# Performance work log

Hardware: AMD Instinct MI355X
Metric: run time of the kernel (lower is better)

Reference implementation:

```python
import jax, jax.numpy as jnp
import numpy as np

B, T, D, H, L, K, DFF = 8, 512, 512, 8, 4, 31, 2048
DK = D // H
PAD = (K - 1) // 2

def _ln(x, g, b, eps=1e-5):
    m = x.mean(-1, keepdims=True)
    v = ((x - m) ** 2).mean(-1, keepdims=True)
    return (x - m) * jax.lax.rsqrt(v + eps) * g + b

def _swish(x):
    return x * jax.nn.sigmoid(x)

def _rel_shift(x):
    # x: [B,H,T,P] with P = 2T-1 (Transformer-XL style shift)
    b, h, q, p = x.shape
    x = jnp.pad(x, ((0, 0), (0, 0), (0, 0), (1, 0)))
    x = x.reshape(b, h, p + 1, q)[:, :, 1:].reshape(b, h, q, p)
    return x

def setup_inputs() -> dict:
    key = jax.random.key(0)
    ks = iter(jax.random.split(key, 64))
    def w(shape, s=0.02):
        return jax.random.normal(next(ks), shape, jnp.float32) * s
    inp = {
        'x': jax.random.normal(next(ks), (B, T, D), jnp.float32),
        'pos_emb': jax.random.normal(next(ks), (1, 2 * T - 1, D), jnp.float32),
        'ln1_g': jnp.ones((L, D)), 'ln1_b': jnp.zeros((L, D)),
        'ff1_w1': w((L, D, DFF)), 'ff1_b1': jnp.zeros((L, DFF)),
        'ff1_w2': w((L, DFF, D)), 'ff1_b2': jnp.zeros((L, D)),
        'lnA_g': jnp.ones((L, D)), 'lnA_b': jnp.zeros((L, D)),
        'Wq': w((L, D, D)), 'bq': jnp.zeros((L, D)),
        'Wk': w((L, D, D)), 'bk': jnp.zeros((L, D)),
        'Wv': w((L, D, D)), 'bv': jnp.zeros((L, D)),
        'Wo': w((L, D, D)), 'bo': jnp.zeros((L, D)),
        'Wpos': w((L, D, D)),
        'pbu': jnp.zeros((L, H, DK)), 'pbv': jnp.zeros((L, H, DK)),
        'lnC_g': jnp.ones((L, D)), 'lnC_b': jnp.zeros((L, D)),
        'pw1_w': w((L, 2 * D, D)), 'pw1_b': jnp.zeros((L, 2 * D)),
        'dw_w': w((L, D, K)), 'dw_b': jnp.zeros((L, D)),
        'cln_g': jnp.ones((L, D)), 'cln_b': jnp.zeros((L, D)),
        'pw2_w': w((L, D, D)), 'pw2_b': jnp.zeros((L, D)),
        'ln2_g': jnp.ones((L, D)), 'ln2_b': jnp.zeros((L, D)),
        'ff2_w1': w((L, D, DFF)), 'ff2_b1': jnp.zeros((L, DFF)),
        'ff2_w2': w((L, DFF, D)), 'ff2_b2': jnp.zeros((L, D)),
        'lnO_g': jnp.ones((L, D)), 'lnO_b': jnp.zeros((L, D)),
    }
    return inp

def reference(x, pos_emb, ln1_g, ln1_b, ff1_w1, ff1_b1, ff1_w2, ff1_b2,
              lnA_g, lnA_b, Wq, bq, Wk, bk, Wv, bv, Wo, bo, Wpos, pbu, pbv,
              lnC_g, lnC_b, pw1_w, pw1_b, dw_w, dw_b, cln_g, cln_b, pw2_w, pw2_b,
              ln2_g, ln2_b, ff2_w1, ff2_b1, ff2_w2, ff2_b2, lnO_g, lnO_b):
    scale = 1.0 / np.sqrt(DK).astype(np.float32)
    for i in range(L):
        # FFN 1 (half-step residual)
        res = x
        y = _ln(x, ln1_g[i], ln1_b[i])
        y = _swish(y @ ff1_w1[i] + ff1_b1[i]) @ ff1_w2[i] + ff1_b2[i]
        res = res + 0.5 * y
        # rel-pos multi-head self-attention
        y = _ln(res, lnA_g[i], lnA_b[i])
        q = (y @ Wq[i] + bq[i]).reshape(B, T, H, DK)
        k = (y @ Wk[i] + bk[i]).reshape(B, T, H, DK)
        v = (y @ Wv[i] + bv[i]).reshape(B, T, H, DK)
        p = (pos_emb @ Wpos[i]).reshape(1, 2 * T - 1, H, DK)
        ac = jnp.einsum('bthd,bshd->bhts', q + pbu[i], k)          # content score
        bd = jnp.einsum('bthd,xshd->bhts', q + pbv[i], p)          # position score
        bd = _rel_shift(bd)[..., :T]
        attn = jax.nn.softmax((ac + bd) * scale, axis=-1)
        o = jnp.einsum('bhts,bshd->bthd', attn, v).reshape(B, T, D)
        res = res + (o @ Wo[i] + bo[i])
        # convolution module
        y = _ln(res, lnC_g[i], lnC_b[i])
        y = y @ pw1_w[i].T + pw1_b[i]                               # (B,T,2D)
        a, g = jnp.split(y, 2, axis=-1)
        y = a * jax.nn.sigmoid(g)                                   # GLU over channels
        y = jax.lax.conv_general_dilated(
            y.transpose(0, 2, 1), dw_w[i][:, None, :],
            window_strides=(1,), padding=[(PAD, PAD)],
            feature_group_count=D,
            dimension_numbers=('NCH', 'OIH', 'NCH'))
        y = y.transpose(0, 2, 1) + dw_b[i]                          # (B,T,D)
        y = _swish(_ln(y, cln_g[i], cln_b[i]))
        y = y @ pw2_w[i].T + pw2_b[i]
        res = res + y
        # FFN 2 (half-step residual)
        y = _ln(res, ln2_g[i], ln2_b[i])
        y = _swish(y @ ff2_w1[i] + ff2_b1[i]) @ ff2_w2[i] + ff2_b2[i]
        res = res + 0.5 * y
        x = _ln(res, lnO_g[i], lnO_b[i])
    return x
```

## Files before the change

kernel.cpp:

```cpp
#include <hip/hip_runtime.h>


typedef unsigned short u16;
typedef unsigned int u32;
typedef __attribute__((ext_vector_type(8))) short bf16x8;
typedef __attribute__((ext_vector_type(4))) float f32x4;

#define DI __device__ __forceinline__

constexpr int CT = 512;
constexpr int CD = 512;
constexpr int CH = 8;
constexpr int CDK = 64;
constexpr int CDFF = 2048;
constexpr int CNBT = 4096;
constexpr int CL = 4;

DI u16 f2bf(float f) {
  u32 u = __builtin_bit_cast(u32, f);
  u = u + 0x7fffu + ((u >> 16) & 1u);
  return (u16)(u >> 16);
}
DI float bf2f(u16 h) { u32 u = ((u32)h) << 16; return __builtin_bit_cast(float, u); }
DI u32 pack2(float a, float b) { return (u32)f2bf(a) | ((u32)f2bf(b) << 16); }
DI float sigm(float x) { return 1.0f / (1.0f + __expf(-x)); }

DI f32x4 MFMA(bf16x8 a, bf16x8 b, f32x4 c) {
  return __builtin_amdgcn_mfma_f32_16x16x32_bf16(a, b, c, 0, 0, 0);
}

DI void gload16(const void* g, void* l) {
  __builtin_amdgcn_global_load_lds((const __attribute__((address_space(1))) void*)g,
                                   (__attribute__((address_space(3))) void*)l, 16, 0, 0);
}

DI float wsum(float v) {
#pragma unroll
  for (int o = 32; o > 0; o >>= 1) v += __shfl_xor(v, o, 64);
  return v;
}

DI void tbody(const float* ip, u16* op, int R, int C, int c0, int r0,
              int tx, int ty) {
  __shared__ float t[32][33];
#pragma unroll
  for (int i = ty; i < 32; i += 8)
    t[i][tx] = ip[(long)(r0 + i) * C + c0 + tx];
  __syncthreads();
#pragma unroll
  for (int i = ty; i < 32; i += 8)
    op[(long)(c0 + i) * R + r0 + tx] = f2bf(t[tx][i]);
}

__global__ __launch_bounds__(256) void tconv2x_k(const float* __restrict__ in0,
                                                 const float* __restrict__ in1,
                                                 u16* __restrict__ out0,
                                                 u16* __restrict__ out1,
                                                 int R, int C) {
  int z = blockIdx.z;
  int l = z & 3;
  const float* ip = (z < 4 ? in0 : in1) + (long)l * R * C;
  u16* op = (z < 4 ? out0 : out1) + (long)l * R * C;
  tbody(ip, op, R, C, blockIdx.x * 32, blockIdx.y * 32, threadIdx.x, threadIdx.y);
}

__global__ __launch_bounds__(256) void tconvQ_k(
    const float* __restrict__ Wq, const float* __restrict__ Wk,
    const float* __restrict__ Wv, const float* __restrict__ Wo,
    const float* __restrict__ Wpos, u16* __restrict__ wt_qkv,
    u16* __restrict__ wt_o, u16* __restrict__ wt_pos) {
  int z = blockIdx.z;
  int sel = z >> 2, l = z & 3;
  const float* ip;
  u16* op;
  const long S = 512L * 512;
  switch (sel) {
    case 0: ip = Wq + l * S; op = wt_qkv + (long)l * 1536 * 512; break;
    case 1: ip = Wk + l * S; op = wt_qkv + (long)l * 1536 * 512 + S; break;
    case 2: ip = Wv + l * S; op = wt_qkv + (long)l * 1536 * 512 + 2 * S; break;
    case 3: ip = Wo + l * S; op = wt_o + l * S; break;
    default: ip = Wpos + l * S; op = wt_pos + l * S; break;
  }
  tbody(ip, op, 512, 512, blockIdx.x * 32, blockIdx.y * 32, threadIdx.x, threadIdx.y);
}

__global__ __launch_bounds__(256) void cvt_k(const float* __restrict__ in,
                                             u16* __restrict__ out, long nIn, long nOut,
                                             long inZ, long outZ) {
  long i = ((long)blockIdx.x * 256 + threadIdx.x) * 4;
  if (i >= nOut) return;
  const float* ip = in + (long)blockIdx.y * inZ;
  u16* op = out + (long)blockIdx.y * outZ;
  u16 o[4];
#pragma unroll
  for (int j = 0; j < 4; ++j) {
    long idx = i + j;
    o[j] = (idx < nIn) ? f2bf(ip[idx]) : (u16)0;
  }
  uint2 st;
  st.x = (u32)o[0] | ((u32)o[1] << 16);
  st.y = (u32)o[2] | ((u32)o[3] << 16);
  *(uint2*)&op[i] = st;
}

__global__ __launch_bounds__(256) void pwperm_k(const float* __restrict__ in,
                                                u16* __restrict__ out) {
  int l = blockIdx.y;
  long i = (long)blockIdx.x * 256 + threadIdx.x;
  long n = i >> 7;
  int c = (int)(i & 127) * 4;
  int q = (int)(n >> 4) & 1;
  long r = (q ? 512 : 0) + ((n >> 5) << 4) + (n & 15);
  const float* ip = in + ((long)l * 1024 + r) * 512 + c;
  float4 v = *(const float4*)ip;
  u16* op = out + ((long)l * 1024 + n) * 512 + c;
  uint2 st;
  st.x = pack2(v.x, v.y);
  st.y = pack2(v.z, v.w);
  *(uint2*)op = st;
}

__global__ __launch_bounds__(256) void setup3_k(
    const float* __restrict__ in_pos, u16* __restrict__ posbf,
    const float* __restrict__ dw_w, float* __restrict__ dwT,
    const float* __restrict__ bq, const float* __restrict__ bk,
    const float* __restrict__ bv, float* __restrict__ qkvb) {
  int y = blockIdx.y;
  long x = blockIdx.x;
  int tid = threadIdx.x;
  if (y == 0) {
    long i = (x * 256 + tid) * 4;
    const long nIn = 1023L * 512, nOut = 1024L * 512;
    if (i >= nOut) return;
    u16 o[4];
#pragma unroll
    for (int j = 0; j < 4; ++j) {
      long idx = i + j;
      o[j] = (idx < nIn) ? f2bf(in_pos[idx]) : (u16)0;
    }
    uint2 st;
    st.x = (u32)o[0] | ((u32)o[1] << 16);
    st.y = (u32)o[2] | ((u32)o[3] << 16);
    *(uint2*)&posbf[i] = st;
  } else if (y == 1) {
    long idx = x * 256 + tid;
    if (idx >= 4L * 31 * 512) return;
    long l = idx / (31 * 512);
    int rem = (int)(idx % (31 * 512));
    int k = rem >> 9, d = rem & 511;
    dwT[idx] = dw_w[l * 512 * 31 + d * 31 + k];
  } else {
    long idx = x * 256 + tid;
    if (idx >= 4L * 1536) return;
    int z = (int)(idx / 1536), j = (int)(idx % 1536);
    float v;
    if (j < 512) v = bq[z * 512 + j];
    else if (j < 1024) v = bk[z * 512 + j - 512];
    else v = bv[z * 512 + j - 1024];
    qkvb[idx] = v;
  }
}

template <int F32OUT>
__global__ __launch_bounds__(256) void ln_k(const float* in, void* out,
                                            const float* gw, const float* bw) {
  int tid = threadIdx.x, wid = tid >> 6, lane = tid & 63;
  long row = (long)blockIdx.x * 4 + wid;
  const float* x = in + row * CD + lane * 8;
  float4 v0 = *(const float4*)x;
  float4 v1 = *(const float4*)(x + 4);
  float s = v0.x + v0.y + v0.z + v0.w + v1.x + v1.y + v1.z + v1.w;
  float q = v0.x * v0.x + v0.y * v0.y + v0.z * v0.z + v0.w * v0.w +
            v1.x * v1.x + v1.y * v1.y + v1.z * v1.z + v1.w * v1.w;
  s = wsum(s);
  q = wsum(q);
  float mean = s * (1.0f / CD);
  float var = q * (1.0f / CD) - mean * mean;
  float rs = rsqrtf(var + 1e-5f);
  int c = lane * 8;
  float4 g0 = *(const float4*)(gw + c), g1 = *(const float4*)(gw + c + 4);
  float4 b0 = *(const float4*)(bw + c), b1 = *(const float4*)(bw + c + 4);
  float y0 = (v0.x - mean) * rs * g0.x + b0.x;
  float y1 = (v0.y - mean) * rs * g0.y + b0.y;
  float y2 = (v0.z - mean) * rs * g0.z + b0.z;
  float y3 = (v0.w - mean) * rs * g0.w + b0.w;
  float y4 = (v1.x - mean) * rs * g1.x + b1.x;
  float y5 = (v1.y - mean) * rs * g1.y + b1.y;
  float y6 = (v1.z - mean) * rs * g1.z + b1.z;
  float y7 = (v1.w - mean) * rs * g1.w + b1.w;
  if (F32OUT) {
    float* o = (float*)out + row * CD + c;
    *(float4*)o = make_float4(y0, y1, y2, y3);
    *(float4*)(o + 4) = make_float4(y4, y5, y6, y7);
  } else {
    u16* o = (u16*)out + row * CD + c;
    uint4 pk;
    pk.x = pack2(y0, y1);
    pk.y = pack2(y2, y3);
    pk.z = pack2(y4, y5);
    pk.w = pack2(y6, y7);
    *(uint4*)o = pk;
  }
}

__global__ __launch_bounds__(256) void ln_cp_k(const float* __restrict__ in,
                                               float* __restrict__ cur,
                                               u16* __restrict__ ybf,
                                               const float* gw, const float* bw) {
  int tid = threadIdx.x, wid = tid >> 6, lane = tid & 63;
  long row = (long)blockIdx.x * 4 + wid;
  const float* x = in + row * CD + lane * 8;
  float v[8];
  *(float4*)&v[0] = *(const float4*)x;
  *(float4*)&v[4] = *(const float4*)(x + 4);
  float* cx = cur + row * CD + lane * 8;
  *(float4*)cx = *(float4*)&v[0];
  *(float4*)(cx + 4) = *(float4*)&v[4];
  float s = 0.f, q = 0.f;
#pragma unroll
  for (int j = 0; j < 8; ++j) { s += v[j]; q += v[j] * v[j]; }
  s = wsum(s);
  q = wsum(q);
  float mean = s * (1.0f / CD);
  float var = q * (1.0f / CD) - mean * mean;
  float rs = rsqrtf(var + 1e-5f);
  int c = lane * 8;
  float y[8];
#pragma unroll
  for (int j = 0; j < 8; ++j) y[j] = (v[j] - mean) * rs * gw[c + j] + bw[c + j];
  u16* o = ybf + row * CD + c;
  uint4 pk;
  pk.x = pack2(y[0], y[1]);
  pk.y = pack2(y[2], y[3]);
  pk.z = pack2(y[4], y[5]);
  pk.w = pack2(y[6], y[7]);
  *(uint4*)o = pk;
}

__global__ __launch_bounds__(256) void lnln_k(float* cur, u16* ybf,
                                              const float* gO, const float* bO,
                                              const float* g1, const float* b1) {
  int tid = threadIdx.x, wid = tid >> 6, lane = tid & 63;
  long row = (long)blockIdx.x * 4 + wid;
  float* x = cur + row * CD + lane * 8;
  float v[8];
  *(float4*)&v[0] = *(const float4*)x;
  *(float4*)&v[4] = *(const float4*)(x + 4);
  float s = 0.f, q = 0.f;
#pragma unroll
  for (int j = 0; j < 8; ++j) { s += v[j]; q += v[j] * v[j]; }
  s = wsum(s);
  q = wsum(q);
  float mean = s * (1.0f / CD);
  float var = q * (1.0f / CD) - mean * mean;
  float rs = rsqrtf(var + 1e-5f);
  int c = lane * 8;
  float y[8];
#pragma unroll
  for (int j = 0; j < 8; ++j) y[j] = (v[j] - mean) * rs * gO[c + j] + bO[c + j];
  *(float4*)x = *(float4*)&y[0];
  *(float4*)(x + 4) = *(float4*)&y[4];
  float s2 = 0.f, q2 = 0.f;
#pragma unroll
  for (int j = 0; j < 8; ++j) { s2 += y[j]; q2 += y[j] * y[j]; }
  s2 = wsum(s2);
  q2 = wsum(q2);
  float mean2 = s2 * (1.0f / CD);
  float var2 = q2 * (1.0f / CD) - mean2 * mean2;
  float rs2 = rsqrtf(var2 + 1e-5f);
  float z[8];
#pragma unroll
  for (int j = 0; j < 8; ++j) z[j] = (y[j] - mean2) * rs2 * g1[c + j] + b1[c + j];
  u16* o = ybf + row * CD + c;
  uint4 pk;
  pk.x = pack2(z[0], z[1]);
  pk.y = pack2(z[2], z[3]);
  pk.z = pack2(z[4], z[5]);
  pk.w = pack2(z[6], z[7]);
  *(uint4*)o = pk;
}

template <int EPI, int SPLITK>
__global__ __launch_bounds__(256, 2) void gemm2_k(
    const u16* __restrict__ A, const u16* __restrict__ B, void* C,
    const float* __restrict__ bias, float alpha, int lda, int ldb, int ldc, int Kd) {
  __shared__ u16 lds[3][2][64 * 64];
  const int tid = threadIdx.x, wid = tid >> 6, lane = tid & 63;
  const int m0 = blockIdx.x * 64, n0 = blockIdx.y * 64;
  const int wm = wid >> 1, wn = wid & 1;
  const int fr = lane & 15, fq = lane >> 4;
  const f32x4 vz = {0.f, 0.f, 0.f, 0.f};
  f32x4 acc[2][2] = {{vz, vz}, {vz, vz}};

  const int Kc = Kd / SPLITK;
  const int kb0 = (SPLITK > 1) ? blockIdx.z * Kc : 0;
  const int nK = Kc / 64;

  auto stage = [&](int buf, int kt) {
    const int k0 = kb0 + kt * 64;
#pragma unroll
    for (int r = 0; r < 2; ++r) {
      int bi = r * 4096 + tid * 16;
      int row = bi >> 7;
      int ch = ((bi >> 4) & 7) ^ (row & 7);
      gload16(A + (long)(m0 + row) * lda + k0 + ch * 8,
              (char*)&lds[buf][0][0] + r * 4096 + wid * 1024);
      gload16(B + (long)(n0 + row) * ldb + k0 + ch * 8,
              (char*)&lds[buf][1][0] + r * 4096 + wid * 1024);
    }
  };

  stage(0, 0);
  if (nK > 1) stage(1, 1);
  for (int kt = 0; kt < nK; ++kt) {
    const int buf = kt % 3;
    if (kt + 1 < nK)
      asm volatile("s_waitcnt vmcnt(4)" ::: "memory");
    else
      asm volatile("s_waitcnt vmcnt(0)" ::: "memory");
    __syncthreads();
    if (kt + 2 < nK) stage((kt + 2) % 3, kt + 2);
    bf16x8 af[2][2], bfv[2][2];
#pragma unroll
    for (int ks = 0; ks < 2; ++ks) {
      int ch = ks * 4 + fq;
#pragma unroll
      for (int i = 0; i < 2; ++i) {
        int arow = wm * 32 + i * 16 + fr;
        af[ks][i] = *(const bf16x8*)((const char*)&lds[buf][0][0] + arow * 128 +
                                     ((ch ^ (arow & 7)) << 4));
        int brow = wn * 32 + i * 16 + fr;
        bfv[ks][i] = *(const bf16x8*)((const char*)&lds[buf][1][0] + brow * 128 +
                                      ((ch ^ (brow & 7)) << 4));
      }
    }
#pragma unroll
    for (int ks = 0; ks < 2; ++ks)
#pragma unroll
      for (int mi = 0; mi < 2; ++mi)
#pragma unroll
        for (int ni = 0; ni < 2; ++ni)
          acc[mi][ni] = MFMA(af[ks][mi], bfv[ks][ni], acc[mi][ni]);
  }

#pragma unroll
  for (int mi = 0; mi < 2; ++mi) {
    const int gmB = m0 + wm * 32 + mi * 16 + fq * 4;
#pragma unroll
    for (int ni = 0; ni < 2; ++ni) {
      const int gn = n0 + wn * 32 + ni * 16 + fr;
      float bv_ = 0.f;
      if constexpr (EPI == 3) bv_ = bias[gn];
#pragma unroll
      for (int r = 0; r < 4; ++r) {
        const int gm = gmB + r;
        float v = acc[mi][ni][r];
        long idx = (long)gm * ldc + gn;
        if constexpr (EPI == 0) ((u16*)C)[idx] = f2bf(v);
        else if constexpr (EPI == 3) {
          float* R = (float*)C;
          if constexpr (SPLITK > 1) {
            float add = alpha * (v + (blockIdx.z == 0 ? bv_ : 0.f));
            atomicAdd(&R[idx], add);
          } else {
            R[idx] += alpha * (v + bv_);
          }
        }
      }
    }
  }
}

template <int EPI>
__global__ __launch_bounds__(256, 2) void gemmB_k(
    const u16* __restrict__ A, const u16* __restrict__ B, void* C,
    u16* __restrict__ Caux, const float* __restrict__ bias,
    int lda, int ldb, int ldc, int Kd) {
  __shared__ u16 ldsA[2][128 * 64];
  __shared__ u16 ldsB[2][128 * 64];
  const int tid = threadIdx.x, wid = tid >> 6, lane = tid & 63;
  const int nwg = gridDim.x * gridDim.y;
  int lin = blockIdx.y * gridDim.x + blockIdx.x;
  lin = (lin & 7) * (nwg >> 3) + (lin >> 3);
  const int m0 = (lin % gridDim.x) * 128, n0 = (lin / gridDim.x) * 128;
  const int wm = wid >> 1, wn = wid & 1;
  const int fr = lane & 15, fq = lane >> 4;
  const f32x4 vz = {0.f, 0.f, 0.f, 0.f};
  f32x4 acc[4][4];
#pragma unroll
  for (int mi = 0; mi < 4; ++mi)
#pragma unroll
    for (int ni = 0; ni < 4; ++ni) acc[mi][ni] = vz;
  const int nK = Kd / 64;

  auto stage = [&](int buf, int kt) {
    const int k0 = kt * 64;
#pragma unroll
    for (int r = 0; r < 4; ++r) {
      int bi = r * 4096 + tid * 16;
      int row = bi >> 7;
      int ch = ((bi >> 4) & 7) ^ (row & 7);
      gload16(A + (long)(m0 + row) * lda + k0 + ch * 8,
              (char*)&ldsA[buf][0] + r * 4096 + wid * 1024);
      gload16(B + (long)(n0 + row) * ldb + k0 + ch * 8,
              (char*)&ldsB[buf][0] + r * 4096 + wid * 1024);
    }
  };

  stage(0, 0);
  asm volatile("s_waitcnt vmcnt(0)" ::: "memory");
  __syncthreads();
  int buf = 0;
  for (int kt = 0; kt < nK; ++kt) {
    if (kt + 1 < nK) stage(buf ^ 1, kt + 1);
#pragma unroll
    for (int ks = 0; ks < 2; ++ks) {
      int ch = ks * 4 + fq;
      bf16x8 af[4], bfv[4];
#pragma unroll
      for (int i = 0; i < 4; ++i) {
        int arow = wm * 64 + i * 16 + fr;
        af[i] = *(const bf16x8*)((const char*)&ldsA[buf][0] + arow * 128 +
                                 ((ch ^ (arow & 7)) << 4));
        int brow = wn * 64 + i * 16 + fr;
        bfv[i] = *(const bf16x8*)((const char*)&ldsB[buf][0] + brow * 128 +
                                  ((ch ^ (brow & 7)) << 4));
      }
#pragma unroll
      for (int mi = 0; mi < 4; ++mi)
#pragma unroll
        for (int ni = 0; ni < 4; ++ni)
          acc[mi][ni] = MFMA(af[mi], bfv[ni], acc[mi][ni]);
    }
    asm volatile("s_waitcnt vmcnt(0)" ::: "memory");
    __syncthreads();
    buf ^= 1;
  }

  if constexpr (EPI == 2) {
#pragma unroll
    for (int mi = 0; mi < 4; ++mi) {
      const int gmB = m0 + wm * 64 + mi * 16 + fq * 4;
#pragma unroll
      for (int ni = 0; ni < 4; ++ni) {
        const int gn = n0 + wn * 64 + ni * 16 + fr;
        float bv_ = bias[gn];
#pragma unroll
        for (int r = 0; r < 4; ++r) {
          float x = acc[mi][ni][r] + bv_;
          ((u16*)C)[(long)(gmB + r) * ldc + gn] = f2bf(x * sigm(x));
        }
      }
    }
  } else if constexpr (EPI == 7) {
#pragma unroll
    for (int mi = 0; mi < 4; ++mi) {
      const int gmB = m0 + wm * 64 + mi * 16 + fq * 4;
#pragma unroll
      for (int p = 0; p < 2; ++p) {
        const int ucol = (n0 >> 1) + wn * 32 + p * 16 + fr;
        float ba = bias[ucol], bg = bias[512 + ucol];
#pragma unroll
        for (int r = 0; r < 4; ++r) {
          float va = acc[mi][2 * p][r] + ba;
          float vg = acc[mi][2 * p + 1][r] + bg;
          ((u16*)C)[(long)(gmB + r) * 512 + ucol] = f2bf(va * sigm(vg));
        }
      }
    }
  } else if constexpr (EPI == 8) {
    if (n0 < 1024) {
#pragma unroll
      for (int mi = 0; mi < 4; ++mi) {
        const int gmB = m0 + wm * 64 + mi * 16 + fq * 4;
#pragma unroll
        for (int ni = 0; ni < 4; ++ni) {
          const int gn = n0 + wn * 64 + ni * 16 + fr;
          float bv_ = bias[gn];
#pragma unroll
          for (int r = 0; r < 4; ++r)
            ((u16*)C)[(long)(gmB + r) * ldc + gn] = f2bf(acc[mi][ni][r] + bv_);
        }
      }
    } else {
#pragma unroll
      for (int mi = 0; mi < 4; ++mi) {
        const int gmB = m0 + wm * 64 + mi * 16 + fq * 4;
        const int b = gmB >> 9, t = gmB & 511;
#pragma unroll
        for (int ni = 0; ni < 4; ++ni) {
          const int gn = n0 + wn * 64 + ni * 16 + fr;
          const int h = (gn - 1024) >> 6, d = (gn - 1024) & 63;
          float bv_ = bias[gn];
          uint2 pk;
          pk.x = pack2(acc[mi][ni][0] + bv_, acc[mi][ni][1] + bv_);
          pk.y = pack2(acc[mi][ni][2] + bv_, acc[mi][ni][3] + bv_);
          *(uint2*)&Caux[((long)(b * 8 + h) * 64 + d) * 512 + t] = pk;
        }
      }
    }
  }
}

__global__ __launch_bounds__(256, 2) void attn_k(
    const u16* __restrict__ qkvp, const u16* __restrict__ pball,
    const float* __restrict__ pbuL, const float* __restrict__ pbvL,
    const u16* __restrict__ vt, u16* __restrict__ out) {
  __shared__ u16 ldsK[2][64 * 64];
  __shared__ u16 ldsP[2][128 * 64];
  __shared__ u16 bd0s[4][16 * 80];
  __shared__ u16 stile[4][16 * 64];
  const int tid = threadIdx.x, wid = tid >> 6, lane = tid & 63;
  const int t0 = blockIdx.x * 64;
  const int bh = blockIdx.y, b = bh >> 3, h = bh & 7;
  const int fr = lane & 15, fq = lane >> 4;

  const u16* kbase = qkvp + (long)(b * CT) * 1536 + 512 + h * 64;
  const u16* pbase = pball + h * 64;
  const float* pu = pbuL + h * 64;
  const float* pv = pbvL + h * 64;

  const u16* qp = qkvp + (long)(b * CT + t0 + wid * 16 + fr) * 1536 + h * 64;
  bf16x8 qua[2], qva[2];
#pragma unroll
  for (int kk = 0; kk < 2; ++kk) {
    bf16x8 qw = *(const bf16x8*)(qp + kk * 32 + fq * 8);
    const float* bu = pu + kk * 32 + fq * 8;
    const float* bv = pv + kk * 32 + fq * 8;
#pragma unroll
    for (int j = 0; j < 8; ++j) {
      float qf = bf2f((u16)qw[j]);
      qua[kk][j] = (short)f2bf(qf + bu[j]);
      qva[kk][j] = (short)f2bf(qf + bv[j]);
    }
  }

  const f32x4 vz = {0.f, 0.f, 0.f, 0.f};
  f32x4 oacc[4] = {vz, vz, vz, vz};
  float m_run[4] = {-1e30f, -1e30f, -1e30f, -1e30f};
  float l_run[4] = {0.f, 0.f, 0.f, 0.f};
  const int jbw = (3 - wid) * 16;

  auto stage = [&](int buf, int st) {
    int s0 = st * 64, j0 = s0 - t0 + 448;
#pragma unroll
    for (int r = 0; r < 2; ++r) {
      int c = r * 256 + tid;
      int row = c >> 3, cs = (c & 7) ^ (row & 7);
      gload16(kbase + (long)(s0 + row) * 1536 + cs * 8,
              (char*)&ldsK[buf][0] + r * 4096 + wid * 1024);
    }
#pragma unroll
    for (int r = 0; r < 4; ++r) {
      int c = r * 256 + tid;
      int row = c >> 3, cs = (c & 7) ^ (row & 7);
      gload16(pbase + (long)(j0 + row) * 2048 + cs * 8,
              (char*)&ldsP[buf][0] + r * 4096 + wid * 1024);
    }
  };

  stage(0, 0);
  int cur = 0;
  for (int st = 0; st < 8; ++st) {
    const int s0 = st * 64;
    if (st + 1 < 8) {
      stage(cur ^ 1, st + 1);
      asm volatile("s_waitcnt vmcnt(6)" ::: "memory");
    } else {
      asm volatile("s_waitcnt vmcnt(0)" ::: "memory");
    }
    __syncthreads();

    bf16x8 vb[4][2];
#pragma unroll
    for (int ni = 0; ni < 4; ++ni)
#pragma unroll
      for (int kk = 0; kk < 2; ++kk)
        vb[ni][kk] = *(const bf16x8*)&vt[((long)bh * 64 + ni * 16 + fr) * 512 +
                                         s0 + kk * 32 + fq * 8];

    __builtin_amdgcn_s_setprio(1);
    f32x4 ac[4] = {vz, vz, vz, vz};
#pragma unroll
    for (int kk = 0; kk < 2; ++kk) {
#pragma unroll
      for (int ni = 0; ni < 4; ++ni) {
        int row = ni * 16 + fr;
        bf16x8 kb = *(const bf16x8*)((const char*)&ldsK[cur][0] +
                                     ((row * 128 + kk * 64 + fq * 16) ^ ((row & 7) << 4)));
        ac[ni] = MFMA(qua[kk], kb, ac[ni]);
      }
    }
    f32x4 bd[5] = {vz, vz, vz, vz, vz};
#pragma unroll
    for (int kk = 0; kk < 2; ++kk) {
#pragma unroll
      for (int nbi = 0; nbi < 5; ++nbi) {
        int row = jbw + nbi * 16 + fr;
        bf16x8 pb = *(const bf16x8*)((const char*)&ldsP[cur][0] +
                                     ((row * 128 + kk * 64 + fq * 16) ^ ((row & 7) << 4)));
        bd[nbi] = MFMA(qva[kk], pb, bd[nbi]);
      }
    }
    __builtin_amdgcn_s_setprio(0);
#pragma unroll
    for (int nbi = 0; nbi < 5; ++nbi)
#pragma unroll
      for (int r = 0; r < 4; ++r)
        bd0s[wid][(fq * 4 + r) * 80 + nbi * 16 + fr] = f2bf(bd[nbi][r]);

    float vals[4][4];
#pragma unroll
    for (int ni = 0; ni < 4; ++ni)
#pragma unroll
      for (int r = 0; r < 4; ++r) {
        int tlw = fq * 4 + r;
        int jcol = ni * 16 + fr + 15 - tlw;
        vals[ni][r] = (ac[ni][r] + bf2f(bd0s[wid][tlw * 80 + jcol])) * 0.125f;
      }
    float scf[4];
#pragma unroll
    for (int r = 0; r < 4; ++r) {
      float mx = fmaxf(fmaxf(vals[0][r], vals[1][r]), fmaxf(vals[2][r], vals[3][r]));
      mx = fmaxf(mx, __shfl_xor(mx, 1));
      mx = fmaxf(mx, __shfl_xor(mx, 2));
      mx = fmaxf(mx, __shfl_xor(mx, 4));
      mx = fmaxf(mx, __shfl_xor(mx, 8));
      float mnew = fmaxf(m_run[r], mx);
      scf[r] = __expf(m_run[r] - mnew);
      m_run[r] = mnew;
      float sum = 0.f;
#pragma unroll
      for (int ni = 0; ni < 4; ++ni) {
        float p = __expf(vals[ni][r] - mnew);
        vals[ni][r] = p;
        sum += p;
      }
      sum += __shfl_xor(sum, 1);
      sum += __shfl_xor(sum, 2);
      sum += __shfl_xor(sum, 4);
      sum += __shfl_xor(sum, 8);
      l_run[r] = l_run[r] * scf[r] + sum;
    }
#pragma unroll
    for (int ni = 0; ni < 4; ++ni)
#pragma unroll
      for (int r = 0; r < 4; ++r) {
        int tlw = fq * 4 + r;
        *(u16*)((char*)&stile[wid][0] +
                (((tlw * 128) + (ni * 16 + fr) * 2) ^ ((tlw & 7) << 4))) =
            f2bf(vals[ni][r]);
      }
#pragma unroll
    for (int ni = 0; ni < 4; ++ni)
#pragma unroll
      for (int r = 0; r < 4; ++r) oacc[ni][r] *= scf[r];
    __builtin_amdgcn_s_setprio(1);
#pragma unroll
    for (int kk = 0; kk < 2; ++kk) {
      bf16x8 pa = *(const bf16x8*)((const char*)&stile[wid][0] +
                                   ((fr * 128 + kk * 64 + fq * 16) ^ ((fr & 7) << 4)));
#pragma unroll
      for (int ni = 0; ni < 4; ++ni) oacc[ni] = MFMA(pa, vb[ni][kk], oacc[ni]);
    }
    __builtin_amdgcn_s_setprio(0);
    __syncthreads();
    cur ^= 1;
  }

  float inv[4];
#pragma unroll
  for (int r = 0; r < 4; ++r) inv[r] = 1.0f / l_run[r];
#pragma unroll
  for (int ni = 0; ni < 4; ++ni)
#pragma unroll
    for (int r = 0; r < 4; ++r) {
      long row = (long)(b * CT + t0 + wid * 16 + fq * 4 + r) * CD + h * CDK;
      out[row + ni * 16 + fr] = f2bf(oacc[ni][r] * inv[r]);
    }
}

__global__ __launch_bounds__(256) void conv2_k(const u16* __restrict__ u,
                                               const float* __restrict__ wT,
                                               const float* __restrict__ wb,
                                               const float* __restrict__ cg,
                                               const float* __restrict__ cb,
                                               u16* __restrict__ out) {
  constexpr int TT = 8;
  int tid = threadIdx.x, d0 = tid * 2;
  int b = blockIdx.y, t0 = blockIdx.x * TT;
  const u16* ub = u + ((long)b * CT) * CD + d0;

  u32 strip[TT + 30];
#pragma unroll
  for (int j = 0; j < TT + 30; ++j) {
    int tt = t0 + j - 15;
    strip[j] = ((unsigned)tt < (unsigned)CT) ? *(const u32*)(ub + (long)tt * CD) : 0u;
  }
  float2 bias = *(const float2*)(wb + d0);
  float a0[TT], a1[TT];
#pragma unroll
  for (int t = 0; t < TT; ++t) { a0[t] = bias.x; a1[t] = bias.y; }
#pragma unroll
  for (int k = 0; k < 31; ++k) {
    float2 wk = *(const float2*)(wT + k * CD + d0);
#pragma unroll
    for (int t = 0; t < TT; ++t) {
      u32 pr = strip[t + k];
      a0[t] += bf2f((u16)(pr & 0xffff)) * wk.x;
      a1[t] += bf2f((u16)(pr >> 16)) * wk.y;
    }
  }
  __shared__ float redS[4][TT], redQ[4][TT];
  int wid = tid >> 6, lane = tid & 63;
#pragma unroll
  for (int t = 0; t < TT; ++t) {
    float s = a0[t] + a1[t];
    float q = a0[t] * a0[t] + a1[t] * a1[t];
    s = wsum(s);
    q = wsum(q);
    if (lane == 0) { redS[wid][t] = s; redQ[wid][t] = q; }
  }
  __syncthreads();
  float2 g2 = *(const float2*)(cg + d0);
  float2 b2 = *(const float2*)(cb + d0);
#pragma unroll
  for (int t = 0; t < TT; ++t) {
    float s = redS[0][t] + redS[1][t] + redS[2][t] + redS[3][t];
    float q = redQ[0][t] + redQ[1][t] + redQ[2][t] + redQ[3][t];
    float mean = s * (1.f / 512), var = q * (1.f / 512) - mean * mean;
    float rs = rsqrtf(var + 1e-5f);
    float y0 = (a0[t] - mean) * rs * g2.x + b2.x;
    float y1 = (a1[t] - mean) * rs * g2.y + b2.y;
    y0 = y0 * sigm(y0);
    y1 = y1 * sigm(y1);
    *(u32*)(out + ((long)(b * CT + t0 + t)) * CD + d0) = pack2(y0, y1);
  }
}

extern "C" void kernel_launch(void* const* d_in, const int* in_sizes, int n_in,
                              void* d_out, int out_size, void* d_ws, size_t ws_size,
                              hipStream_t stream) {
  const float* in_x   = (const float*)d_in[0];
  const float* in_pos = (const float*)d_in[1];
  const float* ln1_g  = (const float*)d_in[2];
  const float* ln1_b  = (const float*)d_in[3];
  const float* ff1_w1 = (const float*)d_in[4];
  const float* ff1_b1 = (const float*)d_in[5];
  const float* ff1_w2 = (const float*)d_in[6];
  const float* ff1_b2 = (const float*)d_in[7];
  const float* lnA_g  = (const float*)d_in[8];
  const float* lnA_b  = (const float*)d_in[9];
  const float* Wq     = (const float*)d_in[10];
  const float* bq     = (const float*)d_in[11];
  const float* Wk     = (const float*)d_in[12];
  const float* bk     = (const float*)d_in[13];
  const float* Wv     = (const float*)d_in[14];
  const float* bv     = (const float*)d_in[15];
  const float* Wo     = (const float*)d_in[16];
  const float* bo     = (const float*)d_in[17];
  const float* Wpos   = (const float*)d_in[18];
  const float* pbu    = (const float*)d_in[19];
  const float* pbv    = (const float*)d_in[20];
  const float* lnC_g  = (const float*)d_in[21];
  const float* lnC_b  = (const float*)d_in[22];
  const float* pw1_w  = (const float*)d_in[23];
  const float* pw1_b  = (const float*)d_in[24];
  const float* dw_w   = (const float*)d_in[25];
  const float* dw_b   = (const float*)d_in[26];
  const float* cln_g  = (const float*)d_in[27];
  const float* cln_b  = (const float*)d_in[28];
  const float* pw2_w  = (const float*)d_in[29];
  const float* pw2_b  = (const float*)d_in[30];
  const float* ln2_g  = (const float*)d_in[31];
  const float* ln2_b  = (const float*)d_in[32];
  const float* ff2_w1 = (const float*)d_in[33];
  const float* ff2_b1 = (const float*)d_in[34];
  const float* ff2_w2 = (const float*)d_in[35];
  const float* ff2_b2 = (const float*)d_in[36];
  const float* lnO_g  = (const float*)d_in[37];
  const float* lnO_b  = (const float*)d_in[38];
  (void)in_sizes; (void)n_in; (void)out_size; (void)ws_size;

  char* ws = (char*)d_ws;
  size_t off = 0;
  auto alloc = [&](size_t bytes) -> void* {
    off = (off + 255) & ~(size_t)255;
    void* p = ws + off;
    off += bytes;
    return p;
  };

  u16* wt_ff1w1 = (u16*)alloc((size_t)CL * CDFF * CD * 2);
  u16* wt_ff1w2 = (u16*)alloc((size_t)CL * CD * CDFF * 2);
  u16* wt_qkv   = (u16*)alloc((size_t)CL * 1536 * CD * 2);
  u16* wt_o     = (u16*)alloc((size_t)CL * CD * CD * 2);
  u16* wt_pos   = (u16*)alloc((size_t)CL * CD * CD * 2);
  u16* w_pw1p   = (u16*)alloc((size_t)CL * 1024 * CD * 2);
  u16* w_pw2    = (u16*)alloc((size_t)CL * CD * CD * 2);
  u16* wt_ff2w1 = (u16*)alloc((size_t)CL * CDFF * CD * 2);
  u16* wt_ff2w2 = (u16*)alloc((size_t)CL * CD * CDFF * 2);
  float* qkvbias = (float*)alloc((size_t)CL * 1536 * 4);
  u16* posbf = (u16*)alloc((size_t)1024 * CD * 2);
  float* dwT = (float*)alloc((size_t)CL * 31 * CD * 4);
  u16* pbf_all = (u16*)alloc((size_t)1024 * 2048 * 2);
  float* cur = (float*)alloc((size_t)CNBT * CD * 4);
  u16* ybf   = (u16*)alloc((size_t)CNBT * CD * 2);
  u16* qkv   = (u16*)alloc((size_t)CNBT * 1536 * 2);
  u16* hbf   = (u16*)alloc((size_t)CNBT * CDFF * 2);
  u16* vt    = (u16*)alloc((size_t)64 * CDK * CT * 2);
  u16* obf   = (u16*)alloc((size_t)CNBT * CD * 2);
  u16* ubuf  = (u16*)alloc((size_t)CNBT * CD * 2);
  u16* cbf   = (u16*)alloc((size_t)CNBT * CD * 2);

  dim3 b256(256);
  dim3 tb(32, 8);

  tconv2x_k<<<dim3(CDFF / 32, CD / 32, 2 * CL), tb, 0, stream>>>(
      ff1_w1, ff2_w1, wt_ff1w1, wt_ff2w1, CD, CDFF);
  tconv2x_k<<<dim3(CD / 32, CDFF / 32, 2 * CL), tb, 0, stream>>>(
      ff1_w2, ff2_w2, wt_ff1w2, wt_ff2w2, CDFF, CD);
  tconvQ_k<<<dim3(CD / 32, CD / 32, 5 * CL), tb, 0, stream>>>(
      Wq, Wk, Wv, Wo, Wpos, wt_qkv, wt_o, wt_pos);
  pwperm_k<<<dim3(512, CL), b256, 0, stream>>>(pw1_w, w_pw1p);
  cvt_k<<<dim3(256, CL, 1), b256, 0, stream>>>(pw2_w, w_pw2, 512L * 512, 512L * 512,
                                               512L * 512, 512L * 512);
  setup3_k<<<dim3(512, 3), b256, 0, stream>>>(in_pos, posbf, dw_w, dwT,
                                              bq, bk, bv, qkvbias);
  ln_cp_k<<<dim3(1024), b256, 0, stream>>>(in_x, cur, ybf, ln1_g, ln1_b);
  gemm2_k<0, 1><<<dim3(16, 32, 1), b256, 0, stream>>>(
      posbf, wt_pos, pbf_all, nullptr, 0.f, CD, CD, 2048, CD);

  for (int i = 0; i < CL; ++i) {
    const u16* Wf1 = wt_ff1w1 + (long)i * CDFF * CD;
    const u16* Wf2 = wt_ff1w2 + (long)i * CD * CDFF;
    const u16* Wqk = wt_qkv + (long)i * 1536 * CD;
    const u16* Wou = wt_o + (long)i * CD * CD;
    const u16* Wp1 = w_pw1p + (long)i * 1024 * CD;
    const u16* Wp2 = w_pw2 + (long)i * CD * CD;
    const u16* Wf3 = wt_ff2w1 + (long)i * CDFF * CD;
    const u16* Wf4 = wt_ff2w2 + (long)i * CD * CDFF;

    gemmB_k<2><<<dim3(32, 16, 1), b256, 0, stream>>>(
        ybf, Wf1, hbf, nullptr, ff1_b1 + (long)i * CDFF, CD, CD, CDFF, CD);
    gemm2_k<3, 1><<<dim3(64, 8, 1), b256, 0, stream>>>(
        hbf, Wf2, cur, ff1_b2 + i * CD, 0.5f, CDFF, CDFF, CD, CDFF);

    ln_k<0><<<dim3(1024), b256, 0, stream>>>(cur, ybf, lnA_g + i * CD, lnA_b + i * CD);
    gemmB_k<8><<<dim3(32, 12, 1), b256, 0, stream>>>(
        ybf, Wqk, qkv, vt, qkvbias + i * 1536, CD, CD, 1536, CD);
    attn_k<<<dim3(8, 64), b256, 0, stream>>>(qkv, pbf_all + i * 512, pbu + i * 512,
                                             pbv + i * 512, vt, obf);
    gemm2_k<3, 1><<<dim3(64, 8, 1), b256, 0, stream>>>(
        obf, Wou, cur, bo + i * CD, 1.0f, CD, CD, CD, CD);

    ln_k<0><<<dim3(1024), b256, 0, stream>>>(cur, ybf, lnC_g + i * CD, lnC_b + i * CD);
    gemmB_k<7><<<dim3(32, 8, 1), b256, 0, stream>>>(
        ybf, Wp1, ubuf, nullptr, pw1_b + (long)i * 1024, CD, CD, 512, CD);
    conv2_k<<<dim3(CT / 8, 8), b256, 0, stream>>>(ubuf, dwT + (long)i * 31 * CD,
                                                  dw_b + i * CD, cln_g + i * CD,
                                                  cln_b + i * CD, cbf);
    gemm2_k<3, 1><<<dim3(64, 8, 1), b256, 0, stream>>>(
        cbf, Wp2, cur, pw2_b + i * CD, 1.0f, CD, CD, CD, CD);

    ln_k<0><<<dim3(1024), b256, 0, stream>>>(cur, ybf, ln2_g + i * CD, ln2_b + i * CD);
    gemmB_k<2><<<dim3(32, 16, 1), b256, 0, stream>>>(
        ybf, Wf3, hbf, nullptr, ff2_b1 + (long)i * CDFF, CD, CD, CDFF, CD);
    gemm2_k<3, 1><<<dim3(64, 8, 1), b256, 0, stream>>>(
        hbf, Wf4, cur, ff2_b2 + i * CD, 0.5f, CDFF, CDFF, CD, CDFF);

    if (i < CL - 1)
      lnln_k<<<dim3(1024), b256, 0, stream>>>(cur, ybf, lnO_g + i * CD, lnO_b + i * CD,
                                              ln1_g + (i + 1) * CD, ln1_b + (i + 1) * CD);
    else
      ln_k<1><<<dim3(1024), b256, 0, stream>>>(cur, d_out, lnO_g + i * CD, lnO_b + i * CD);
  }
}
```

Before: 771.1 us.

## Triple-buffer big GEMM with BK=32 and raise occupancy to 3 waves

```diff
diff --git a/kernel.cpp b/kernel.cpp
--- a/kernel.cpp
+++ b/kernel.cpp
@@ -281,7 +281,7 @@
 }
 
 template <int EPI, int SPLITK>
-__global__ __launch_bounds__(256, 2) void gemm2_k(
+__global__ __launch_bounds__(256, 3) void gemm2_k(
     const u16* __restrict__ A, const u16* __restrict__ B, void* C,
     const float* __restrict__ bias, float alpha, int lda, int ldb, int ldc, int Kd) {
   __shared__ u16 lds[3][2][64 * 64];
@@ -315,10 +315,10 @@
   for (int kt = 0; kt < nK; ++kt) {
     const int buf = kt % 3;
     if (kt + 1 < nK)
-      asm volatile("s_waitcnt vmcnt(4)" ::: "memory");
+      asm volatile("s_waitcnt vmcnt(4) lgkmcnt(0)" ::: "memory");
     else
-      asm volatile("s_waitcnt vmcnt(0)" ::: "memory");
-    __syncthreads();
+      asm volatile("s_waitcnt vmcnt(0) lgkmcnt(0)" ::: "memory");
+    __builtin_amdgcn_s_barrier();
     if (kt + 2 < nK) stage((kt + 2) % 3, kt + 2);
     bf16x8 af[2][2], bfv[2][2];
 #pragma unroll
@@ -372,12 +372,12 @@
 }
 
 template <int EPI>
-__global__ __launch_bounds__(256, 2) void gemmB_k(
+__global__ __launch_bounds__(256, 3) void gemmB_k(
     const u16* __restrict__ A, const u16* __restrict__ B, void* C,
     u16* __restrict__ Caux, const float* __restrict__ bias,
     int lda, int ldb, int ldc, int Kd) {
-  __shared__ u16 ldsA[2][128 * 64];
-  __shared__ u16 ldsB[2][128 * 64];
+  __shared__ u16 ldsA[3][128 * 32];
+  __shared__ u16 ldsB[3][128 * 32];
   const int tid = threadIdx.x, wid = tid >> 6, lane = tid & 63;
   const int nwg = gridDim.x * gridDim.y;
   int lin = blockIdx.y * gridDim.x + blockIdx.x;
@@ -391,50 +391,53 @@
   for (int mi = 0; mi < 4; ++mi)
 #pragma unroll
     for (int ni = 0; ni < 4; ++ni) acc[mi][ni] = vz;
-  const int nK = Kd / 64;
+  const int nK = Kd / 32;
 
   auto stage = [&](int buf, int kt) {
-    const int k0 = kt * 64;
-#pragma unroll
-    for (int r = 0; r < 4; ++r) {
+    const int k0 = kt * 32;
+#pragma unroll
+    for (int r = 0; r < 2; ++r) {
       int bi = r * 4096 + tid * 16;
-      int row = bi >> 7;
-      int ch = ((bi >> 4) & 7) ^ (row & 7);
-      gload16(A + (long)(m0 + row) * lda + k0 + ch * 8,
+      int sr = bi >> 7;
+      int cc = ((bi >> 4) & 7) ^ (sr & 7);
+      int row = 2 * sr + (cc >> 2);
+      int kc = cc & 3;
+      gload16(A + (long)(m0 + row) * lda + k0 + kc * 8,
               (char*)&ldsA[buf][0] + r * 4096 + wid * 1024);
-      gload16(B + (long)(n0 + row) * ldb + k0 + ch * 8,
+      gload16(B + (long)(n0 + row) * ldb + k0 + kc * 8,
               (char*)&ldsB[buf][0] + r * 4096 + wid * 1024);
     }
   };
 
   stage(0, 0);
-  asm volatile("s_waitcnt vmcnt(0)" ::: "memory");
-  __syncthreads();
-  int buf = 0;
+  if (nK > 1) stage(1, 1);
   for (int kt = 0; kt < nK; ++kt) {
-    if (kt + 1 < nK) stage(buf ^ 1, kt + 1);
-#pragma unroll
-    for (int ks = 0; ks < 2; ++ks) {
-      int ch = ks * 4 + fq;
-      bf16x8 af[4], bfv[4];
-#pragma unroll
-      for (int i = 0; i < 4; ++i) {
-        int arow = wm * 64 + i * 16 + fr;
-        af[i] = *(const bf16x8*)((const char*)&ldsA[buf][0] + arow * 128 +
-                                 ((ch ^ (arow & 7)) << 4));
-        int brow = wn * 64 + i * 16 + fr;
-        bfv[i] = *(const bf16x8*)((const char*)&ldsB[buf][0] + brow * 128 +
-                                  ((ch ^ (brow & 7)) << 4));
-      }
-#pragma unroll
-      for (int mi = 0; mi < 4; ++mi)
-#pragma unroll
-        for (int ni = 0; ni < 4; ++ni)
-          acc[mi][ni] = MFMA(af[mi], bfv[ni], acc[mi][ni]);
-    }
-    asm volatile("s_waitcnt vmcnt(0)" ::: "memory");
-    __syncthreads();
-    buf ^= 1;
+    const int buf = kt % 3;
+    if (kt + 1 < nK)
+      asm volatile("s_waitcnt vmcnt(4) lgkmcnt(0)" ::: "memory");
+    else
+      asm volatile("s_waitcnt vmcnt(0) lgkmcnt(0)" ::: "memory");
+    __builtin_amdgcn_s_barrier();
+    if (kt + 2 < nK) stage((kt + 2) % 3, kt + 2);
+    bf16x8 af[4], bfv[4];
+#pragma unroll
+    for (int i = 0; i < 4; ++i) {
+      int arow = wm * 64 + i * 16 + fr;
+      int srA = arow >> 1;
+      int ccA = ((arow & 1) << 2) | fq;
+      af[i] = *(const bf16x8*)((const char*)&ldsA[buf][0] + srA * 128 +
+                               ((ccA ^ (srA & 7)) << 4));
+      int brow = wn * 64 + i * 16 + fr;
+      int srB = brow >> 1;
+      int ccB = ((brow & 1) << 2) | fq;
+      bfv[i] = *(const bf16x8*)((const char*)&ldsB[buf][0] + srB * 128 +
+                                ((ccB ^ (srB & 7)) << 4));
+    }
+#pragma unroll
+    for (int mi = 0; mi < 4; ++mi)
+#pragma unroll
+      for (int ni = 0; ni < 4; ++ni)
+        acc[mi][ni] = MFMA(af[mi], bfv[ni], acc[mi][ni]);
   }
 
   if constexpr (EPI == 2) {
```

Result: no change. 777.3 us (+0.8%).
